# Performance work log

Hardware: AMD Instinct MI355X
Metric: run time of the kernel (lower is better)

## Reference

```python
import jax, jax.numpy as jnp
import numpy as np

TEMPERATURE = 0.7
BIG_NEG = -1e30  # safe stand-in for -inf (keeps grads finite)


def setup_inputs() -> dict:
    key = jax.random.key(0)
    k1, k2, k3 = jax.random.split(key, 3)
    B, D = 8192, 256
    embeddings = jax.random.normal(k1, (B, D), dtype=jnp.float32)
    categories = jax.random.randint(k2, (B,), 0, 16, dtype=jnp.int64)
    font_labels = jax.random.randint(k3, (B,), 0, 2000, dtype=jnp.int64)
    return {"embeddings": embeddings, "categories": categories, "font_labels": font_labels}


def reference(embeddings, categories, font_labels):
    # L2-normalize rows
    e = embeddings / jnp.linalg.norm(embeddings, axis=1, keepdims=True)
    sims = jnp.matmul(e, e.T) / TEMPERATURE  # [B, B]
    B = sims.shape[0]

    same = categories[:, None] == categories[None, :]
    diag = jnp.eye(B, dtype=bool)
    pos_mask = same & ~diag           # same category, excluding self
    neg_mask = ~same                  # different category (self excluded implicitly)

    valid = pos_mask.any(axis=1) & neg_mask.any(axis=1)

    pos_sim = jnp.max(jnp.where(pos_mask, sims, BIG_NEG), axis=1)  # hardest positive per anchor
    neg_max = jnp.max(jnp.where(neg_mask, sims, BIG_NEG), axis=1)

    # logsumexp over {pos_sim} U neg_sims, numerically stable
    m = jnp.where(valid, jnp.maximum(pos_sim, neg_max), 0.0)
    pos_safe = jnp.where(valid, pos_sim, 0.0)
    exp_neg_sum = jnp.sum(jnp.where(neg_mask, jnp.exp(sims - m[:, None]), 0.0), axis=1)
    lse = m + jnp.log(jnp.exp(pos_safe - m) + exp_neg_sum)

    loss_per_anchor = -pos_safe + lse
    n_valid = jnp.maximum(jnp.sum(valid), 1)
    return jnp.sum(jnp.where(valid, loss_per_anchor, 0.0)) / n_valid
```

## Files before the change

kernel.cpp:

```cpp
#include <hip/hip_runtime.h>
#include <stdint.h>

#define NROWS 8192
#define DDIM 256
#define NSTRIPS 32
#define STRIP_COLS 256
#define BN 32
#define NTILES 8
#define BM 256
#define NSLOT NSTRIPS

#define ESCALE 1.4356159f
#define LN2F   0.6931471806f
#define NEGBIG (-1e30f)

typedef __attribute__((ext_vector_type(8))) short short8;
typedef __attribute__((ext_vector_type(4))) float f32x4;

typedef __attribute__((address_space(3))) void lds_void;
typedef const __attribute__((address_space(1))) void gl_void;

__device__ __forceinline__ unsigned short f2bf(float x) {
  unsigned int u = __float_as_uint(x);
  u += 0x7fffu + ((u >> 16) & 1u);
  return (unsigned short)(u >> 16);
}

__global__ __launch_bounds__(256) void knorm(const float* __restrict__ emb,
                                             unsigned short* __restrict__ ebf,
                                             uint4* __restrict__ accv) {
  if (blockIdx.x == 0 && threadIdx.x == 0) *accv = (uint4){0u, 0u, 0u, 0u};
  const int wave = threadIdx.x >> 6, lane = threadIdx.x & 63;
  const int row = blockIdx.x * 4 + wave;
  const float4 v = *(const float4*)(emb + row * DDIM + lane * 4);
  float ss = v.x * v.x + v.y * v.y + v.z * v.z + v.w * v.w;
#pragma unroll
  for (int off = 1; off < 64; off <<= 1) ss += __shfl_xor(ss, off, 64);
  const float sc = rsqrtf(ss) * ESCALE;
  ushort4 o;
  o.x = f2bf(v.x * sc); o.y = f2bf(v.y * sc);
  o.z = f2bf(v.z * sc); o.w = f2bf(v.w * sc);
  *(ushort4*)(ebf + row * DDIM + lane * 4) = o;
}

__global__ __launch_bounds__(512) void kmain(const unsigned short* __restrict__ ebf,
                                             const int* __restrict__ cats,
                                             float* __restrict__ posP,
                                             float* __restrict__ sumP) {
  __shared__ alignas(16) unsigned short smem[2][BN * DDIM];
  const int tid = threadIdx.x;
  const int lane = tid & 63, wave = tid >> 6;
  const int lane15 = lane & 15, quad = lane >> 4;
  const int strip = blockIdx.x, rowTile = blockIdx.y;
  const int rowG = rowTile * BM + wave * 32;
  const int col0 = strip * STRIP_COLS;

  short8 a[2][8];
#pragma unroll
  for (int m = 0; m < 2; ++m)
#pragma unroll
    for (int kk = 0; kk < 8; ++kk)
      a[m][kk] = *(const short8*)(ebf + (rowG + m * 16 + lane15) * DDIM + kk * 32 + quad * 8);

  int cati[2][4];
#pragma unroll
  for (int m = 0; m < 2; ++m)
#pragma unroll
    for (int r = 0; r < 4; ++r)
      cati[m][r] = cats[rowG + m * 16 + quad * 4 + r];

  bool dlr[4];
#pragma unroll
  for (int r = 0; r < 4; ++r) dlr[r] = (lane15 == quad * 4 + r);

  float pm[2][4], ns[2][4];
#pragma unroll
  for (int m = 0; m < 2; ++m)
#pragma unroll
    for (int r = 0; r < 4; ++r) { pm[m][r] = NEGBIG; ns[m][r] = 0.f; }

#define STAGE(t, buf)                                                           \
  {                                                                             \
    const unsigned short* g = ebf +                                             \
        (size_t)(col0 + (t) * BN + (lane & 31)) * DDIM +                        \
        (wave * 2 + (lane >> 5)) * 8;                                           \
    char* lb = (char*)&smem[(buf)][0] + wave * 1024;                            \
    _Pragma("unroll")                                                           \
    for (int c = 0; c < 2; ++c)                                                 \
      __builtin_amdgcn_global_load_lds((gl_void*)(g + c * 128),                 \
                                       (lds_void*)(lb + c * 8192), 16, 0, 0);   \
  }

  STAGE(0, 0);

  for (int t = 0; t < NTILES; ++t) {
    __syncthreads();
    if (t + 1 < NTILES) STAGE(t + 1, (t + 1) & 1);
    const char* bb = (const char*)&smem[t & 1][0];
    const int colBase = col0 + t * BN;
    const int cjt[2] = {cats[colBase + lane15], cats[colBase + 16 + lane15]};

#pragma unroll
    for (int nt = 0; nt < 2; ++nt) {
      short8 b[8];
#pragma unroll
      for (int kk = 0; kk < 8; ++kk)
        b[kk] = *(const short8*)(bb + kk * 2048 + quad * 512 + nt * 256 + lane15 * 16);
      f32x4 acc0 = {0.f, 0.f, 0.f, 0.f}, acc1 = {0.f, 0.f, 0.f, 0.f};
      __builtin_amdgcn_s_setprio(1);
#pragma unroll
      for (int kk = 0; kk < 8; ++kk) {
        acc0 = __builtin_amdgcn_mfma_f32_16x16x32_bf16(a[0][kk], b[kk], acc0, 0, 0, 0);
        acc1 = __builtin_amdgcn_mfma_f32_16x16x32_bf16(a[1][kk], b[kk], acc1, 0, 0, 0);
      }
      __builtin_amdgcn_s_setprio(0);
      const int cj = cjt[nt];
      const bool dg0 = (rowG == colBase + nt * 16);
      const bool dg1 = (rowG + 16 == colBase + nt * 16);
#pragma unroll
      for (int m = 0; m < 2; ++m) {
        const bool dg = m ? dg1 : dg0;
#pragma unroll
        for (int r = 0; r < 4; ++r) {
          const float s = m ? acc1[r] : acc0[r];
          const float e = __builtin_amdgcn_exp2f(s);
          const bool same = (cj == cati[m][r]);
          float psv = same ? s : NEGBIG;
          if (dg) psv = dlr[r] ? NEGBIG : psv;
          pm[m][r] = fmaxf(pm[m][r], psv);
          ns[m][r] += same ? 0.f : e;
        }
      }
    }
  }

#pragma unroll
  for (int off = 1; off < 16; off <<= 1) {
#pragma unroll
    for (int m = 0; m < 2; ++m)
#pragma unroll
      for (int r = 0; r < 4; ++r) {
        pm[m][r] = fmaxf(pm[m][r], __shfl_xor(pm[m][r], off, 64));
        ns[m][r] += __shfl_xor(ns[m][r], off, 64);
      }
  }
  if (lane15 == 0) {
#pragma unroll
    for (int m = 0; m < 2; ++m)
#pragma unroll
      for (int r = 0; r < 4; ++r) {
        const int row = rowG + m * 16 + quad * 4 + r;
        posP[strip * NROWS + row] = pm[m][r];
        sumP[strip * NROWS + row] = ns[m][r];
      }
  }
}

__global__ __launch_bounds__(256) void kmerge(const float* __restrict__ posP,
                                              const float* __restrict__ sumP,
                                              float* __restrict__ acc,
                                              float* __restrict__ out) {
  const int row = blockIdx.x * 256 + threadIdx.x;
  float pm = NEGBIG, ns = 0.f;
#pragma unroll 8
  for (int s = 0; s < NSLOT; ++s) {
    pm = fmaxf(pm, posP[s * NROWS + row]);
    ns += sumP[s * NROWS + row];
  }
  const bool valid = (pm > -1e29f) && (ns > 0.f);
  float loss = valid ? (logf(__builtin_amdgcn_exp2f(pm) + ns) - pm * LN2F) : 0.f;
  float cnt = valid ? 1.f : 0.f;
#pragma unroll
  for (int off = 1; off < 64; off <<= 1) {
    loss += __shfl_xor(loss, off, 64);
    cnt += __shfl_xor(cnt, off, 64);
  }
  if ((threadIdx.x & 63) == 0) {
    atomicAdd(&acc[0], loss);
    atomicAdd(&acc[1], cnt);
    __threadfence();
  }
  __syncthreads();
  if (threadIdx.x == 0) {
    const int prev = atomicAdd((int*)(acc + 2), 1);
    if (prev == (int)gridDim.x - 1) {
      const float L = atomicAdd(&acc[0], 0.f);
      const float C = atomicAdd(&acc[1], 0.f);
      out[0] = L / fmaxf(C, 1.f);
    }
  }
}

extern "C" void kernel_launch(void* const* d_in, const int* in_sizes, int n_in,
                              void* d_out, int out_size, void* d_ws, size_t ws_size,
                              hipStream_t stream) {
  const float* emb = (const float*)d_in[0];
  const int* cats = (const int*)d_in[1];
  float* out = (float*)d_out;

  char* ws = (char*)d_ws;
  float* accv = (float*)ws;
  unsigned short* ebf = (unsigned short*)(ws + 256);
  float* posP = (float*)(ws + 256 + NROWS * DDIM * 2);
  float* sumP = posP + NSLOT * NROWS;

  knorm<<<NROWS / 4, 256, 0, stream>>>(emb, ebf, (uint4*)ws);
  kmain<<<dim3(NSTRIPS, NROWS / BM), 512, 0, stream>>>(ebf, cats, posP, sumP);
  kmerge<<<NROWS / 256, 256, 0, stream>>>(posP, sumP, accv, out);
}
```

Before: 127.5 us.

## Load B operands directly from a pre-swizzled global copy instead of LDS staging

The normalize kernel now also writes a second, MFMA-fragment-ordered copy of the bf16 embeddings. The main kernel loads B fragments straight from global memory (relying on L2/L1) and drops the LDS double-buffer along with its block barriers. The block is halved to 4 waves and 128 rows, which doubles the grid. This removes the LDS staging and synchronisation overhead, at the cost of an extra 4MB write and more global/cache traffic per block.

```diff
diff --git a/kernel.cpp b/kernel.cpp
--- a/kernel.cpp
+++ b/kernel.cpp
@@ -7,7 +7,7 @@
 #define STRIP_COLS 256
 #define BN 32
 #define NTILES 8
-#define BM 256
+#define BM 128
 #define NSLOT NSTRIPS
 
 #define ESCALE 1.4356159f
@@ -17,9 +17,6 @@
 typedef __attribute__((ext_vector_type(8))) short short8;
 typedef __attribute__((ext_vector_type(4))) float f32x4;
 
-typedef __attribute__((address_space(3))) void lds_void;
-typedef const __attribute__((address_space(1))) void gl_void;
-
 __device__ __forceinline__ unsigned short f2bf(float x) {
   unsigned int u = __float_as_uint(x);
   u += 0x7fffu + ((u >> 16) & 1u);
@@ -28,6 +25,7 @@
 
 __global__ __launch_bounds__(256) void knorm(const float* __restrict__ emb,
                                              unsigned short* __restrict__ ebf,
+                                             unsigned short* __restrict__ ebfB,
                                              uint4* __restrict__ accv) {
   if (blockIdx.x == 0 && threadIdx.x == 0) *accv = (uint4){0u, 0u, 0u, 0u};
   const int wave = threadIdx.x >> 6, lane = threadIdx.x & 63;
@@ -41,13 +39,14 @@
   o.x = f2bf(v.x * sc); o.y = f2bf(v.y * sc);
   o.z = f2bf(v.z * sc); o.w = f2bf(v.w * sc);
   *(ushort4*)(ebf + row * DDIM + lane * 4) = o;
+  *(ushort4*)(ebfB + ((lane >> 1) * NROWS + row) * 8 + (lane & 1) * 4) = o;
 }
 
-__global__ __launch_bounds__(512) void kmain(const unsigned short* __restrict__ ebf,
+__global__ __launch_bounds__(256) void kmain(const unsigned short* __restrict__ ebf,
+                                             const unsigned short* __restrict__ ebfB,
                                              const int* __restrict__ cats,
                                              float* __restrict__ posP,
                                              float* __restrict__ sumP) {
-  __shared__ alignas(16) unsigned short smem[2][BN * DDIM];
   const int tid = threadIdx.x;
   const int lane = tid & 63, wave = tid >> 6;
   const int lane15 = lane & 15, quad = lane >> 4;
@@ -79,33 +78,16 @@
 #pragma unroll
     for (int r = 0; r < 4; ++r) { pm[m][r] = NEGBIG; ns[m][r] = 0.f; }
 
-#define STAGE(t, buf)                                                           \
-  {                                                                             \
-    const unsigned short* g = ebf +                                             \
-        (size_t)(col0 + (t) * BN + (lane & 31)) * DDIM +                        \
-        (wave * 2 + (lane >> 5)) * 8;                                           \
-    char* lb = (char*)&smem[(buf)][0] + wave * 1024;                            \
-    _Pragma("unroll")                                                           \
-    for (int c = 0; c < 2; ++c)                                                 \
-      __builtin_amdgcn_global_load_lds((gl_void*)(g + c * 128),                 \
-                                       (lds_void*)(lb + c * 8192), 16, 0, 0);   \
-  }
-
-  STAGE(0, 0);
+  const unsigned short* bbase = ebfB + ((size_t)quad * NROWS + col0 + lane15) * 8;
 
   for (int t = 0; t < NTILES; ++t) {
-    __syncthreads();
-    if (t + 1 < NTILES) STAGE(t + 1, (t + 1) & 1);
-    const char* bb = (const char*)&smem[t & 1][0];
-    const int colBase = col0 + t * BN;
-    const int cjt[2] = {cats[colBase + lane15], cats[colBase + 16 + lane15]};
-
 #pragma unroll
     for (int nt = 0; nt < 2; ++nt) {
+      const int colBase = col0 + t * BN + nt * 16;
       short8 b[8];
 #pragma unroll
       for (int kk = 0; kk < 8; ++kk)
-        b[kk] = *(const short8*)(bb + kk * 2048 + quad * 512 + nt * 256 + lane15 * 16);
+        b[kk] = *(const short8*)(bbase + ((size_t)kk * 4 * NROWS + t * BN + nt * 16) * 8);
       f32x4 acc0 = {0.f, 0.f, 0.f, 0.f}, acc1 = {0.f, 0.f, 0.f, 0.f};
       __builtin_amdgcn_s_setprio(1);
 #pragma unroll
@@ -114,9 +96,9 @@
         acc1 = __builtin_amdgcn_mfma_f32_16x16x32_bf16(a[1][kk], b[kk], acc1, 0, 0, 0);
       }
       __builtin_amdgcn_s_setprio(0);
-      const int cj = cjt[nt];
-      const bool dg0 = (rowG == colBase + nt * 16);
-      const bool dg1 = (rowG + 16 == colBase + nt * 16);
+      const int cj = cats[colBase + lane15];
+      const bool dg0 = (rowG == colBase);
+      const bool dg1 = (rowG + 16 == colBase);
 #pragma unroll
       for (int m = 0; m < 2; ++m) {
         const bool dg = m ? dg1 : dg0;
@@ -201,10 +183,11 @@
   char* ws = (char*)d_ws;
   float* accv = (float*)ws;
   unsigned short* ebf = (unsigned short*)(ws + 256);
-  float* posP = (float*)(ws + 256 + NROWS * DDIM * 2);
+  unsigned short* ebfB = ebf + (size_t)NROWS * DDIM;
+  float* posP = (float*)(ws + 256 + 2 * (size_t)NROWS * DDIM * 2);
   float* sumP = posP + NSLOT * NROWS;
 
-  knorm<<<NROWS / 4, 256, 0, stream>>>(emb, ebf, (uint4*)ws);
-  kmain<<<dim3(NSTRIPS, NROWS / BM), 512, 0, stream>>>(ebf, cats, posP, sumP);
+  knorm<<<NROWS / 4, 256, 0, stream>>>(emb, ebf, ebfB, (uint4*)ws);
+  kmain<<<dim3(NSTRIPS, NROWS / BM), 256, 0, stream>>>(ebf, ebfB, cats, posP, sumP);
   kmerge<<<NROWS / 256, 256, 0, stream>>>(posP, sumP, accv, out);
 }
```

Result: faster. 121.1 us (-5.0%).
